# Optimization experiments

Hardware: AMD Instinct MI355X
Metric: run time of the kernel (lower is better)

## Reference

```python
import math
import jax, jax.numpy as jnp
import numpy as np

H = 16          # num attention heads
D = 64          # head dim
BUCKETS = 256   # position_buckets
MAX_POS = 512   # max_relative_positions
ATT_SPAN = BUCKETS  # pos_ebd_size A
SCALE_FACTOR = 3    # 1 + len(['c2p','p2c'])


def _log_bucket(rel):
    # log-bucketed relative positions (DeBERTa-v2 _make_log_bucket_position)
    mid = BUCKETS // 2
    rel = jnp.clip(rel, -MAX_POS + 1, MAX_POS - 1)
    sign = jnp.sign(rel).astype(jnp.float32)
    abs_pos = jnp.maximum(jnp.abs(rel), 1)
    log_base = math.log((MAX_POS - 1) / mid)
    log_pos = jnp.ceil(jnp.log(abs_pos.astype(jnp.float32) / mid) / log_base * (mid - 1)) + mid
    bucket = jnp.where(abs_pos < mid, abs_pos.astype(jnp.float32), log_pos) * sign
    return bucket.astype(jnp.int32)


def _rel_pos(q_len, k_len):
    q = jnp.arange(q_len, dtype=jnp.int32)
    k = jnp.arange(k_len, dtype=jnp.int32)
    return _log_bucket(q[:, None] - k[None, :])  # (Q, K)


def setup_inputs() -> dict:
    key = jax.random.key(0)
    ks = jax.random.split(key, 6)
    B, S, Hd = 4, 1024, 1024
    std = 0.02
    return {
        "hidden_states": jax.random.normal(ks[0], (B, S, Hd), jnp.float32),
        "rel_embeddings": jax.random.normal(ks[1], (2 * ATT_SPAN, Hd), jnp.float32) * std,
        "Wq": jax.random.normal(ks[2], (Hd, H * D), jnp.float32) * std,
        "bq": jnp.zeros((H * D,), jnp.float32),
        "Wk": jax.random.normal(ks[3], (Hd, H * D), jnp.float32) * std,
        "bk": jnp.zeros((H * D,), jnp.float32),
        "Wv": jax.random.normal(ks[4], (Hd, H * D), jnp.float32) * std,
        "bv": jnp.zeros((H * D,), jnp.float32),
    }


def reference(hidden_states, rel_embeddings, Wq, bq, Wk, bk, Wv, bv):
    B, S, Hd = hidden_states.shape
    A2 = 2 * ATT_SPAN

    def heads(x):  # (B,S,H*D) -> (B,H,S,D)
        return x.reshape(B, S, H, D).transpose(0, 2, 1, 3)

    q = heads(hidden_states @ Wq + bq)
    k = heads(hidden_states @ Wk + bk)
    v = heads(hidden_states @ Wv + bv)

    scale = math.sqrt(D * SCALE_FACTOR)
    scores = jnp.einsum('bhqd,bhkd->bhqk', q, k) / scale  # (B,H,S,S)

    rel = _rel_pos(S, S)  # (S,S) int32 bucketed relative ids
    # share_att_key=True: pos key/query use key_proj/query_proj
    pos_k = (rel_embeddings @ Wk + bk).reshape(A2, H, D).transpose(1, 0, 2)  # (H,2A,D)
    pos_q = (rel_embeddings @ Wq + bq).reshape(A2, H, D).transpose(1, 0, 2)  # (H,2A,D)

    # c2p: content->position
    c2p = jnp.einsum('bhqd,hkd->bhqk', q, pos_k)  # (B,H,S,2A)
    c2p_idx = jnp.clip(rel + ATT_SPAN, 0, A2 - 1)  # (S,S)
    c2p = jnp.take_along_axis(c2p, jnp.broadcast_to(c2p_idx[None, None], (B, H, S, S)), axis=-1) / scale

    # p2c: position->content
    p2c = jnp.einsum('bhkd,hqd->bhkq', k, pos_q)  # (B,H,S,2A)
    p2c_idx = jnp.clip(-rel + ATT_SPAN, 0, A2 - 1)  # (S,S)
    p2c = jnp.take_along_axis(p2c, jnp.broadcast_to(p2c_idx[None, None], (B, H, S, S)), axis=-1)
    p2c = jnp.swapaxes(p2c, -1, -2) / scale

    probs = jax.nn.softmax(scores + c2p + p2c, axis=-1)
    ctx = jnp.einsum('bhqk,bhkd->bhqd', probs, v)  # (B,H,S,D)
    return ctx.transpose(0, 2, 1, 3).reshape(B, S, H * D)
```

## Files before the change

### kernel.cpp

```cpp
#include <hip/hip_runtime.h>
#include <hip/hip_bf16.h>
#include <math.h>

typedef __attribute__((ext_vector_type(8))) short v8s;
typedef __attribute__((ext_vector_type(4))) short v4sh;
typedef __attribute__((ext_vector_type(4))) unsigned short v4us;
typedef __attribute__((ext_vector_type(4))) float v4f;
typedef __attribute__((ext_vector_type(4))) int   v4i;

#define AS1(p) ((const __attribute__((address_space(1))) void*)(p))
#define AS3(p) ((__attribute__((address_space(3))) void*)(p))

__device__ inline unsigned short f2b(float f){
  __hip_bfloat16 h = __float2bfloat16(f);
  return __builtin_bit_cast(unsigned short, h);
}
__device__ inline float b2f(unsigned short u){
  __hip_bfloat16 h = __builtin_bit_cast(__hip_bfloat16, u);
  return __bfloat162float(h);
}
__device__ inline unsigned cvtpk(float lo, float hi){
  unsigned d;
  asm("v_cvt_pk_bf16_f32 %0, %1, %2" : "=v"(d) : "v"(lo), "v"(hi));
  return d;
}

__device__ inline int bucket_id(int i){
  int r = i - 1023;
  if (r > 511) r = 511; if (r < -511) r = -511;
  float sign = (r > 0) ? 1.f : ((r < 0) ? -1.f : 0.f);
  int ap = r < 0 ? -r : r; if (ap < 1) ap = 1;
  float bucket;
  if (ap < 128) bucket = (float)ap * sign;
  else {
    float lp = ceilf(logf((float)ap / 128.f) / logf(511.f/128.f) * 127.f) + 128.f;
    bucket = lp * sign;
  }
  int idx = (int)bucket + 256;
  if (idx < 0) idx = 0; if (idx > 511) idx = 511;
  return idx;
}

__global__ __launch_bounds__(256) void pack_x(const float* __restrict__ hs,
                                              const float* __restrict__ rel,
                                              const float* __restrict__ Wq,
                                              const float* __restrict__ Wk,
                                              const float* __restrict__ Wv,
                                              unsigned short* __restrict__ X,
                                              unsigned short* __restrict__ Wt3,
                                              short* __restrict__ tab,
                                              unsigned long long* __restrict__ tab64){
  __shared__ unsigned short t[64][65];
  int blk = blockIdx.x;
  if (blk < 2304){
    const int HT8 = 4096*1024/8;
    int i8 = blk*256 + threadIdx.x;
    const float* src = (i8 < HT8) ? (hs + (size_t)i8*8) : (rel + ((size_t)i8 - HT8)*8);
    v8s o;
    #pragma unroll
    for (int j = 0; j < 8; j++) o[j] = (short)f2b(src[j]);
    *(v8s*)&X[(size_t)i8*8] = o;
    return;
  }
  if (blk < 2313){
    int i = (blk - 2304)*256 + threadIdx.x;
    if (i < 2047) tab[i] = (short)bucket_id(i);
    if (i < 2056){
      unsigned long long w = 0;
      #pragma unroll
      for (int r = 0; r < 4; r++)
        w |= (unsigned long long)(unsigned short)bucket_id(i + r) << (16*r);
      tab64[i] = w;
    }
    return;
  }
  int tb = blk - 2313;
  int wsel = tb >> 8, bx = tb & 255;
  const float* in = (wsel == 0) ? Wq : ((wsel == 1) ? Wk : Wv);
  unsigned short* outp = Wt3 + ((size_t)wsel << 20);
  int r0 = (bx >> 4) << 6, c0 = (bx & 15) << 6;
  int tx = threadIdx.x & 63, ty = threadIdx.x >> 6;
  #pragma unroll
  for (int p = 0; p < 16; p++){ int r = (p<<2)+ty; t[tx][r] = f2b(in[(size_t)(r0+r)*1024 + c0+tx]); }
  __syncthreads();
  #pragma unroll
  for (int p = 0; p < 16; p++){ int c = (p<<2)+ty; outp[(size_t)(c0+c)*1024 + r0+tx] = t[c][tx]; }
}

__global__ __launch_bounds__(256) void gemm_qkv(
    const unsigned short* __restrict__ A,
    const unsigned short* __restrict__ Bt3,
    unsigned short* __restrict__ Qa, unsigned short* __restrict__ Ka,
    unsigned short* __restrict__ VtT,
    const float* __restrict__ bq, const float* __restrict__ bk,
    const float* __restrict__ bv, float alpha_q)
{
  __shared__ unsigned short smem[2*128*64];
  unsigned short* a_tile = smem;
  unsigned short* b_tile = smem + 128*64;
  int nb = (blockIdx.x & 7)*108 + (blockIdx.x >> 3);
  int bm = nb / 24, bn = nb % 24;
  int m0 = bm << 7, n0 = bn << 7;
  int tid = threadIdx.x, lane = tid & 63, wave = tid >> 6;
  int l15 = lane & 15, lhi = lane >> 4;
  int rbase = (wave >> 1) << 6, cbase = (wave & 1) << 6;
  int crow[4], csw[4];
  #pragma unroll
  for (int u = 0; u < 4; u++){
    int ch = tid + (u << 8);
    crow[u] = ch >> 3;
    csw[u] = ((ch & 7) ^ (crow[u] & 7)) << 3;
  }
  v4f acc[4][4] = {};
  for (int kt = 0; kt < 1024; kt += 64){
    #pragma unroll
    for (int u = 0; u < 4; u++){
      int ch = tid + (u << 8);
      __builtin_amdgcn_global_load_lds(AS1(A   + (size_t)(m0 + crow[u])*1024 + kt + csw[u]),
                                       AS3(a_tile + (size_t)ch*8), 16, 0, 0);
      __builtin_amdgcn_global_load_lds(AS1(Bt3 + (size_t)(n0 + crow[u])*1024 + kt + csw[u]),
                                       AS3(b_tile + (size_t)ch*8), 16, 0, 0);
    }
    __syncthreads();
    #pragma unroll
    for (int ks = 0; ks < 2; ks++){
      v8s af[4], bfr[4];
      int kb = (ks << 2) + lhi;
      #pragma unroll
      for (int i = 0; i < 4; i++){
        int r = rbase + (i << 4) + l15;
        af[i] = *(const v8s*)&a_tile[r*64 + ((kb ^ (r & 7)) << 3)];
      }
      #pragma unroll
      for (int j = 0; j < 4; j++){
        int r = cbase + (j << 4) + l15;
        bfr[j] = *(const v8s*)&b_tile[r*64 + ((kb ^ (r & 7)) << 3)];
      }
      #pragma unroll
      for (int i = 0; i < 4; i++)
        #pragma unroll
        for (int j = 0; j < 4; j++)
          acc[i][j] = __builtin_amdgcn_mfma_f32_16x16x32_bf16(af[i], bfr[j], acc[i][j], 0, 0, 0);
    }
    __syncthreads();
  }
  int seg = n0 >> 10;
  int nn0 = n0 & 1023;
  if (seg == 2){
    if (m0 >= 4096) return;
    int bb = m0 >> 10, s0 = m0 & 1023;
    #pragma unroll
    for (int i = 0; i < 4; i++){
      int r = rbase + (i << 4) + (lhi << 2);
      #pragma unroll
      for (int j = 0; j < 4; j++){
        int c = cbase + (j << 4) + l15;
        float bvv = bv[nn0 + c];
        #pragma unroll
        for (int rr = 0; rr < 4; rr++)
          smem[c*128 + ((r + rr) ^ ((c & 7) << 4))] = f2b(acc[i][j][rr] + bvv);
      }
    }
    __syncthreads();
    int v = tid >> 3, sc = (tid & 7) << 4;
    #pragma unroll
    for (int vb = 0; vb < 4; vb++){
      int vv = v + (vb << 5);
      #pragma unroll
      for (int c2 = 0; c2 < 2; c2++){
        int sb = sc + (c2 << 3);
        v8s val = *(const v8s*)&smem[vv*128 + (sb ^ ((vv & 7) << 4))];
        *(v8s*)&VtT[((size_t)(bb << 10) + nn0 + vv)*1024 + s0 + sb] = val;
      }
    }
    return;
  }
  unsigned short* C = (seg == 0) ? Qa : Ka;
  const float* bias = (seg == 0) ? bq : bk;
  float alpha = (seg == 0) ? alpha_q : 1.f;
  #pragma unroll
  for (int i = 0; i < 4; i++){
    int row = rbase + (i << 4) + (lhi << 2);
    #pragma unroll
    for (int j = 0; j < 4; j++){
      int col = cbase + (j << 4) + l15;
      float bvv = bias[nn0 + col];
      #pragma unroll
      for (int r = 0; r < 4; r++)
        smem[(row + r)*128 + (col ^ (((row + r) & 7) << 4))] = f2b((acc[i][j][r] + bvv) * alpha);
    }
  }
  __syncthreads();
  #pragma unroll
  for (int c = 0; c < 8; c++){
    int row = (tid >> 4) + (c << 4);
    int col8 = (tid & 15) << 3;
    v8s val = *(const v8s*)&smem[row*128 + (col8 ^ ((row & 7) << 4))];
    *(v8s*)&C[(size_t)(m0 + row)*1024 + nn0 + col8] = val;
  }
}

__global__ __launch_bounds__(256) void gemm_pos(
    const unsigned short* __restrict__ Qa,
    const unsigned short* __restrict__ Ka,
    unsigned short* __restrict__ C2P,
    unsigned short* __restrict__ P2C)
{
  __shared__ unsigned short smem[2*128*64];
  unsigned short* a_tile = smem;
  unsigned short* b_tile = smem + 128*64;
  int tab = blockIdx.y >> 4, h = blockIdx.y & 15;
  int bm = blockIdx.x >> 2, bn = blockIdx.x & 3;
  int m0 = bm << 7, n0 = bn << 7;
  const unsigned short* A  = tab ? Ka : Qa;
  const unsigned short* Bt = tab ? Qa : Ka;
  unsigned short* C = tab ? P2C : C2P;
  int tid = threadIdx.x, lane = tid & 63, wave = tid >> 6;
  int l15 = lane & 15, lhi = lane >> 4;
  int rbase = (wave >> 1) << 6, cbase = (wave & 1) << 6;
  #pragma unroll
  for (int u = 0; u < 4; u++){
    int ch = tid + (u << 8);
    int row = ch >> 3;
    int csw = ((ch & 7) ^ (row & 7)) << 3;
    __builtin_amdgcn_global_load_lds(AS1(A  + (size_t)(m0 + row)*1024 + (h << 6) + csw),
                                     AS3(a_tile + (size_t)ch*8), 16, 0, 0);
    __builtin_amdgcn_global_load_lds(AS1(Bt + (size_t)(4096 + n0 + row)*1024 + (h << 6) + csw),
                                     AS3(b_tile + (size_t)ch*8), 16, 0, 0);
  }
  __syncthreads();
  v4f acc[4][4] = {};
  #pragma unroll
  for (int ks = 0; ks < 2; ks++){
    v8s af[4], bfr[4];
    int kb = (ks << 2) + lhi;
    #pragma unroll
    for (int i = 0; i < 4; i++){
      int r = rbase + (i << 4) + l15;
      af[i] = *(const v8s*)&a_tile[r*64 + ((kb ^ (r & 7)) << 3)];
    }
    #pragma unroll
    for (int j = 0; j < 4; j++){
      int r = cbase + (j << 4) + l15;
      bfr[j] = *(const v8s*)&b_tile[r*64 + ((kb ^ (r & 7)) << 3)];
    }
    #pragma unroll
    for (int i = 0; i < 4; i++)
      #pragma unroll
      for (int j = 0; j < 4; j++)
        acc[i][j] = __builtin_amdgcn_mfma_f32_16x16x32_bf16(af[i], bfr[j], acc[i][j], 0, 0, 0);
  }
  __syncthreads();
  #pragma unroll
  for (int i = 0; i < 4; i++){
    int row = rbase + (i << 4) + (lhi << 2);
    #pragma unroll
    for (int j = 0; j < 4; j++){
      int col = cbase + (j << 4) + l15;
      #pragma unroll
      for (int r = 0; r < 4; r++)
        smem[(row + r)*128 + (col ^ (((row + r) & 7) << 4))] = f2b(acc[i][j][r]);
    }
  }
  __syncthreads();
  #pragma unroll
  for (int c = 0; c < 8; c++){
    int row = (tid >> 4) + (c << 4);
    int col8 = (tid & 15) << 3;
    v8s val = *(const v8s*)&smem[row*128 + (col8 ^ ((row & 7) << 4))];
    *(v8s*)&C[(size_t)(m0 + row)*8192 + (h << 9) + n0 + col8] = val;
  }
}

__global__ __launch_bounds__(256) void attn(
  const unsigned short* __restrict__ Qall,
  const unsigned short* __restrict__ Kall,
  const unsigned short* __restrict__ Vt,
  const unsigned short* __restrict__ c2p,
  const unsigned short* __restrict__ p2c,
  const short* __restrict__ idxt,
  const unsigned long long* __restrict__ t64g,
  float* __restrict__ out)
{
  __shared__ unsigned short k_lds[64*64];
  __shared__ unsigned short v_lds[64*64];
  __shared__ unsigned short cw[64*72];
  __shared__ unsigned short pw[64*72];
  __shared__ short basc[16*64];
  __shared__ short basp[16*64];

  int bid = blockIdx.x;
  int xcd = bid & 7, jj = bid >> 3;
  int bh = (xcd << 3) + (jj >> 4), qb = jj & 15;
  int b = bh >> 4, h = bh & 15;
  int q0 = qb << 6;
  int tid = threadIdx.x, lane = tid & 63, wave = tid >> 6;
  int l15 = lane & 15, lhi = lane >> 4;

  #pragma unroll
  for (int v = 0; v < 8; v++){
    int i = tid + (v << 8);
    int kt = (i >> 6) & 15, row = i & 63;
    if (i < 1024){
      int bc = idxt[q0 + row - (kt << 6) + 960] & ~7;
      basc[(kt << 6) + row] = (short)(row*72 - bc);
    } else {
      int bp = idxt[q0 + 1023 - (kt << 6) - row] & ~7;
      basp[(kt << 6) + row] = (short)(row*72 - bp);
    }
  }

  int qrow = q0 + (wave << 4) + l15;
  v8s aq[2];
  #pragma unroll
  for (int ks = 0; ks < 2; ks++)
    aq[ks] = *(const v8s*)&Qall[(size_t)((b << 10) + qrow)*1024 + (h << 6) + (ks << 5) + (lhi << 3)];

  int prow_[3], pcc_[3]; bool pval[3];
  #pragma unroll
  for (int u = 0; u < 3; u++){
    int pp = tid + (u << 8);
    pval[u] = pp < 576;
    prow_[u] = pp / 9; pcc_[u] = pp - prow_[u]*9;
  }
  const size_t cbase0 = ((size_t)((b << 10) + q0))*8192 + (h << 9);
  const size_t pbase0 = ((size_t)(b << 10))*8192 + (h << 9);

  unsigned long long t64u[4];

  auto issue_kwin = [&](int kt){
    int k0 = kt << 6;
    #pragma unroll
    for (int u = 0; u < 2; u++){
      int ch = tid + (u << 8);
      int rr = ch >> 3, seg = ch & 7;
      int csw = (seg ^ (rr & 7)) << 3;
      __builtin_amdgcn_global_load_lds(AS1(Kall + (size_t)((b << 10) + k0 + rr)*1024 + (h << 6) + csw),
                                       AS3(k_lds + (size_t)ch*8), 16, 0, 0);
    }
    #pragma unroll
    for (int u = 0; u < 3; u++){
      if (pval[u]){
        int row = prow_[u], cc = pcc_[u];
        int bc = row*72 - (int)basc[(kt << 6) + row];
        __builtin_amdgcn_global_load_lds(AS1(c2p + cbase0 + (size_t)row*8192 + bc + (cc << 3)),
                                         AS3(cw + (size_t)(tid + (u << 8))*8), 16, 0, 0);
      int bp = row*72 - (int)basp[(kt << 6) + row];
        __builtin_amdgcn_global_load_lds(AS1(p2c + pbase0 + (size_t)(k0 + row)*8192 + bp + (cc << 3)),
                                         AS3(pw + (size_t)(tid + (u << 8))*8), 16, 0, 0);
      }
    }
  };
  auto issue_tv = [&](int kt){
    int k0 = kt << 6;
    int Bc = q0 - k0 + (wave << 4) + l15 - (lhi << 2) + 1020;
    #pragma unroll
    for (int j = 0; j < 4; j++) t64u[j] = t64g[Bc - (j << 4)];
    __builtin_amdgcn_sched_barrier(0);
    #pragma unroll
    for (int u = 0; u < 2; u++){
      int ch = tid + (u << 8);
      int rr = ch >> 3, seg = ch & 7;
      int csw = (seg ^ (rr & 7)) << 3;
      __builtin_amdgcn_global_load_lds(AS1(Vt + (size_t)((b << 10) + (h << 6) + rr)*1024 + k0 + csw),
                                       AS3(v_lds + (size_t)ch*8), 16, 0, 0);
    }
  };

  v4f o_acc[4] = {};
  float m_run = -INFINITY, l_part = 0.f;

  __syncthreads();
  issue_kwin(0);
  __builtin_amdgcn_sched_barrier(0);
  issue_tv(0);

  for (int kt = 0; kt < 16; kt++){
    asm volatile("s_waitcnt vmcnt(6)" ::: "memory");
    __builtin_amdgcn_sched_barrier(0);
    __builtin_amdgcn_s_barrier();
    __builtin_amdgcn_sched_barrier(0);

    v4f s_acc[4] = {};
    #pragma unroll
    for (int j = 0; j < 4; j++){
      int krow = (j << 4) + l15;
      #pragma unroll
      for (int ks = 0; ks < 2; ks++){
        v8s kf = *(const v8s*)&k_lds[krow*64 + ((((ks << 2) + lhi) ^ (krow & 7)) << 3)];
        s_acc[j] = __builtin_amdgcn_mfma_f32_16x16x32_bf16(kf, aq[ks], s_acc[j], 0, 0, 0);
      }
    }
    int cvq = (int)basc[(kt << 6) + (wave << 4) + l15];
    #pragma unroll
    for (int j = 0; j < 4; j++){
      v4sh bp4 = *(const v4sh*)&basp[(kt << 6) + (j << 4) + (lhi << 2)];
      v4us idv = __builtin_bit_cast(v4us, t64u[j]);
      #pragma unroll
      for (int r = 0; r < 4; r++){
        int id = (int)idv[3 - r];
        s_acc[j][r] += b2f(cw[cvq + id]) + b2f(pw[(int)bp4[r] + id]);
      }
    }
    float lmax = s_acc[0][0];
    #pragma unroll
    for (int j = 0; j < 4; j++)
      #pragma unroll
      for (int r = 0; r < 4; r++) lmax = fmaxf(lmax, s_acc[j][r]);
    if (__any(lmax > m_run + 6.f)){
      float mx = lmax;
      mx = fmaxf(mx, __shfl_xor(mx, 16));
      mx = fmaxf(mx, __shfl_xor(mx, 32));
      float mnew = fmaxf(m_run, mx);
      float corr = exp2f(m_run - mnew);
      m_run = mnew;
      l_part *= corr;
      float co[4];
      #pragma unroll
      for (int r = 0; r < 4; r++) co[r] = __shfl(corr, (lhi << 2) + r);
      #pragma unroll
      for (int j = 0; j < 4; j++)
        #pragma unroll
        for (int r = 0; r < 4; r++) o_acc[j][r] *= co[r];
    }
    unsigned wj[4][2];
    float ps = 0.f;
    #pragma unroll
    for (int j = 0; j < 4; j++){
      float p0 = exp2f(s_acc[j][0] - m_run);
      float p1 = exp2f(s_acc[j][1] - m_run);
      float p2 = exp2f(s_acc[j][2] - m_run);
      float p3 = exp2f(s_acc[j][3] - m_run);
      ps += (p0 + p1) + (p2 + p3);
      wj[j][0] = cvtpk(p0, p1);
      wj[j][1] = cvtpk(p2, p3);
    }
    l_part += ps;
    #pragma unroll
    for (int p = 0; p < 2; p++){
      asm("v_permlane32_swap_b32 %0, %1" : "+v"(wj[0][p]), "+v"(wj[1][p]));
      asm("v_permlane32_swap_b32 %0, %1" : "+v"(wj[2][p]), "+v"(wj[3][p]));
      asm("v_permlane16_swap_b32 %0, %1" : "+v"(wj[0][p]), "+v"(wj[1][p]));
      asm("v_permlane16_swap_b32 %0, %1" : "+v"(wj[2][p]), "+v"(wj[3][p]));
    }
    v4i pai0 = { (int)wj[0][0], (int)wj[0][1], (int)wj[1][0], (int)wj[1][1] };
    v4i pai1 = { (int)wj[2][0], (int)wj[2][1], (int)wj[3][0], (int)wj[3][1] };
    v8s pa0 = __builtin_bit_cast(v8s, pai0);
    v8s pa1 = __builtin_bit_cast(v8s, pai1);

    asm volatile("s_waitcnt vmcnt(0)" ::: "memory");
    __builtin_amdgcn_sched_barrier(0);
    __builtin_amdgcn_s_barrier();
    __builtin_amdgcn_sched_barrier(0);

    if (kt < 15) issue_kwin(kt + 1);
    __builtin_amdgcn_sched_barrier(0);

    #pragma unroll
    for (int j = 0; j < 4; j++){
      int vrow = (j << 4) + l15;
      v8s vb0 = *(const v8s*)&v_lds[vrow*64 + (((lhi) ^ (vrow & 7)) << 3)];
      o_acc[j] = __builtin_amdgcn_mfma_f32_16x16x32_bf16(pa0, vb0, o_acc[j], 0, 0, 0);
      v8s vb1 = *(const v8s*)&v_lds[vrow*64 + (((4 + lhi) ^ (vrow & 7)) << 3)];
      o_acc[j] = __builtin_amdgcn_mfma_f32_16x16x32_bf16(pa1, vb1, o_acc[j], 0, 0, 0);
    }
    if (kt < 15){
      asm volatile("s_waitcnt lgkmcnt(0)" ::: "memory");
      __builtin_amdgcn_sched_barrier(0);
      __builtin_amdgcn_s_barrier();
      __builtin_amdgcn_sched_barrier(0);
      issue_tv(kt + 1);
    }
  }
  float ls = l_part;
  ls += __shfl_xor(ls, 16);
  ls += __shfl_xor(ls, 32);
  float inv = 1.f / ls;
  float io[4];
  #pragma unroll
  for (int r = 0; r < 4; r++) io[r] = __shfl(inv, (lhi << 2) + r);
  #pragma unroll
  for (int r = 0; r < 4; r++){
    int row = q0 + (wave << 4) + (lhi << 2) + r;
    #pragma unroll
    for (int j = 0; j < 4; j++)
      out[(size_t)((b << 10) + row)*1024 + (h << 6) + (j << 4) + l15] = o_acc[j][r] * io[r];
  }
}

extern "C" void kernel_launch(void* const* d_in, const int* in_sizes, int n_in,
                              void* d_out, int out_size, void* d_ws, size_t ws_size,
                              hipStream_t stream)
{
  const float* hs  = (const float*)d_in[0];
  const float* rel = (const float*)d_in[1];
  const float* Wq  = (const float*)d_in[2];
  const float* bq  = (const float*)d_in[3];
  const float* Wk  = (const float*)d_in[4];
  const float* bk  = (const float*)d_in[5];
  const float* Wv  = (const float*)d_in[6];
  const float* bv  = (const float*)d_in[7];
  float* out = (float*)d_out;

  char* ws = (char*)d_ws;
  size_t off = 0;
  auto alloc = [&](size_t bytes) -> void* {
    void* p = ws + off; off += (bytes + 255) & ~(size_t)255; return p;
  };
  short*              idxt  = (short*)             alloc(2047 * 2);
  unsigned long long* tab64 = (unsigned long long*)alloc(2056 * 8);
  unsigned short* Xb   = (unsigned short*)alloc((size_t)4608*1024*2);
  unsigned short* Wt3  = (unsigned short*)alloc((size_t)3072*1024*2);
  unsigned short* Qa   = (unsigned short*)alloc((size_t)4608*1024*2);
  unsigned short* Ka   = (unsigned short*)alloc((size_t)4608*1024*2);
  unsigned short* VtT  = (unsigned short*)alloc((size_t)4096*1024*2);
  unsigned short* C2P  = (unsigned short*)alloc((size_t)4096*8192*2);
  unsigned short* P2C  = (unsigned short*)alloc((size_t)4096*8192*2);
  (void)                                  alloc(4096);
  (void)ws_size; (void)in_sizes; (void)n_in; (void)out_size;

  pack_x<<<3081, 256, 0, stream>>>(hs, rel, Wq, Wk, Wv, Xb, Wt3, idxt, tab64);

  const float alpha_q = 1.4426950408889634f / sqrtf(192.f);
  gemm_qkv<<<864, 256, 0, stream>>>(Xb, Wt3, Qa, Ka, VtT, bq, bk, bv, alpha_q);

  gemm_pos<<<dim3(128, 32), 256, 0, stream>>>(Qa, Ka, C2P, P2C);

  attn<<<1024, 256, 0, stream>>>(Qa, Ka, VtT, C2P, P2C, idxt, tab64, out);
}
```

Measured before the change: 158.5 us.

## Skip unused pos-GEMM tiles, widen attention blocks to 128 queries, double-buffer V

gemm_pos now returns early for output tiles whose columns fall outside the bucket-index range that the attention kernel will read, and its block order is remapped across XCDs. The attention kernel moves to 512 threads covering 128 query rows, so each K/V tile and p2c window is shared by twice as many queries. V is double-buffered so its load for the next step is issued together with the K/c2p/p2c loads, which removes one barrier per iteration. MFMA sections are wrapped with s_setprio. The risks are lower occupancy from the larger LDS footprint and fewer blocks, plus correctness depending on the skip bounds derived from idxt.

```diff
diff --git a/kernel.cpp b/kernel.cpp
--- a/kernel.cpp
+++ b/kernel.cpp
@@ -203,15 +203,24 @@
 __global__ __launch_bounds__(256) void gemm_pos(
     const unsigned short* __restrict__ Qa,
     const unsigned short* __restrict__ Ka,
+    const short* __restrict__ idxt,
     unsigned short* __restrict__ C2P,
     unsigned short* __restrict__ P2C)
 {
   __shared__ unsigned short smem[2*128*64];
   unsigned short* a_tile = smem;
   unsigned short* b_tile = smem + 128*64;
+  int xs = (blockIdx.x & 7)*16 + (blockIdx.x >> 3);
   int tab = blockIdx.y >> 4, h = blockIdx.y & 15;
-  int bm = blockIdx.x >> 2, bn = blockIdx.x & 3;
+  int bm = xs >> 2, bn = xs & 3;
   int m0 = bm << 7, n0 = bn << 7;
+  {
+    int s0 = m0 & 1023;
+    int lo, hi;
+    if (tab == 0){ lo = idxt[s0];       hi = idxt[s0 + 1150]; }
+    else         { lo = idxt[896 - s0]; hi = idxt[2046 - s0]; }
+    if (n0 > hi + 7 || n0 + 127 < (lo & ~7)) return;
+  }
   const unsigned short* A  = tab ? Ka : Qa;
   const unsigned short* Bt = tab ? Qa : Ka;
   unsigned short* C = tab ? P2C : C2P;
@@ -272,7 +281,7 @@
   }
 }
 
-__global__ __launch_bounds__(256) void attn(
+__global__ __launch_bounds__(512) void attn(
   const unsigned short* __restrict__ Qall,
   const unsigned short* __restrict__ Kall,
   const unsigned short* __restrict__ Vt,
@@ -283,30 +292,32 @@
   float* __restrict__ out)
 {
   __shared__ unsigned short k_lds[64*64];
-  __shared__ unsigned short v_lds[64*64];
-  __shared__ unsigned short cw[64*72];
-  __shared__ unsigned short pw[64*72];
-  __shared__ short basc[16*64];
+  __shared__ unsigned short v_lds[2][64*64];
+  __shared__ unsigned short cw[128*72];
+  __shared__ unsigned short pw[64*152];
+  __shared__ short basc[16*128];
   __shared__ short basp[16*64];
 
   int bid = blockIdx.x;
   int xcd = bid & 7, jj = bid >> 3;
-  int bh = (xcd << 3) + (jj >> 4), qb = jj & 15;
+  int bh = (xcd << 3) + (jj >> 3), qb = jj & 7;
   int b = bh >> 4, h = bh & 15;
-  int q0 = qb << 6;
+  int q0 = qb << 7;
   int tid = threadIdx.x, lane = tid & 63, wave = tid >> 6;
   int l15 = lane & 15, lhi = lane >> 4;
 
   #pragma unroll
-  for (int v = 0; v < 8; v++){
-    int i = tid + (v << 8);
-    int kt = (i >> 6) & 15, row = i & 63;
-    if (i < 1024){
+  for (int v = 0; v < 6; v++){
+    int i = tid + (v << 9);
+    if (i < 2048){
+      int kt = i >> 7, row = i & 127;
       int bc = idxt[q0 + row - (kt << 6) + 960] & ~7;
-      basc[(kt << 6) + row] = (short)(row*72 - bc);
-    } else {
+      basc[i] = (short)(row*72 - bc);
+    } else if (i < 3072){
+      int i2 = i - 2048;
+      int kt = i2 >> 6, row = i2 & 63;
       int bp = idxt[q0 + 1023 - (kt << 6) - row] & ~7;
-      basp[(kt << 6) + row] = (short)(row*72 - bp);
+      basp[i2] = (short)(row*152 - bp);
     }
   }
 
@@ -316,13 +327,6 @@
   for (int ks = 0; ks < 2; ks++)
     aq[ks] = *(const v8s*)&Qall[(size_t)((b << 10) + qrow)*1024 + (h << 6) + (ks << 5) + (lhi << 3)];
 
-  int prow_[3], pcc_[3]; bool pval[3];
-  #pragma unroll
-  for (int u = 0; u < 3; u++){
-    int pp = tid + (u << 8);
-    pval[u] = pp < 576;
-    prow_[u] = pp / 9; pcc_[u] = pp - prow_[u]*9;
-  }
   const size_t cbase0 = ((size_t)((b << 10) + q0))*8192 + (h << 9);
   const size_t pbase0 = ((size_t)(b << 10))*8192 + (h << 9);
 
@@ -330,40 +334,44 @@
 
   auto issue_kwin = [&](int kt){
     int k0 = kt << 6;
-    #pragma unroll
-    for (int u = 0; u < 2; u++){
-      int ch = tid + (u << 8);
-      int rr = ch >> 3, seg = ch & 7;
+    {
+      int rr = tid >> 3, seg = tid & 7;
       int csw = (seg ^ (rr & 7)) << 3;
       __builtin_amdgcn_global_load_lds(AS1(Kall + (size_t)((b << 10) + k0 + rr)*1024 + (h << 6) + csw),
-                                       AS3(k_lds + (size_t)ch*8), 16, 0, 0);
+                                       AS3(k_lds + (size_t)tid*8), 16, 0, 0);
     }
     #pragma unroll
     for (int u = 0; u < 3; u++){
-      if (pval[u]){
-        int row = prow_[u], cc = pcc_[u];
-        int bc = row*72 - (int)basc[(kt << 6) + row];
+      int pp = tid + (u << 9);
+      if (pp < 1152){
+        int row = pp / 9, cc = pp - row*9;
+        int bc = row*72 - (int)basc[(kt << 7) + row];
         __builtin_amdgcn_global_load_lds(AS1(c2p + cbase0 + (size_t)row*8192 + bc + (cc << 3)),
-                                         AS3(cw + (size_t)(tid + (u << 8))*8), 16, 0, 0);
-      int bp = row*72 - (int)basp[(kt << 6) + row];
+                                         AS3(cw + (size_t)pp*8), 16, 0, 0);
+      }
+    }
+    #pragma unroll
+    for (int u = 0; u < 3; u++){
+      int pp = tid + (u << 9);
+      if (pp < 1152){
+        int row = pp / 18, cc = pp - row*18;
+        int bp = row*152 - (int)basp[(kt << 6) + row];
         __builtin_amdgcn_global_load_lds(AS1(p2c + pbase0 + (size_t)(k0 + row)*8192 + bp + (cc << 3)),
-                                         AS3(pw + (size_t)(tid + (u << 8))*8), 16, 0, 0);
+                                         AS3(pw + (size_t)(row*152 + (cc << 3))), 16, 0, 0);
       }
     }
   };
-  auto issue_tv = [&](int kt){
+  auto issue_tv = [&](int kt, int sel){
     int k0 = kt << 6;
     int Bc = q0 - k0 + (wave << 4) + l15 - (lhi << 2) + 1020;
     #pragma unroll
     for (int j = 0; j < 4; j++) t64u[j] = t64g[Bc - (j << 4)];
     __builtin_amdgcn_sched_barrier(0);
-    #pragma unroll
-    for (int u = 0; u < 2; u++){
-      int ch = tid + (u << 8);
-      int rr = ch >> 3, seg = ch & 7;
+    {
+      int rr = tid >> 3, seg = tid & 7;
       int csw = (seg ^ (rr & 7)) << 3;
       __builtin_amdgcn_global_load_lds(AS1(Vt + (size_t)((b << 10) + (h << 6) + rr)*1024 + k0 + csw),
-                                       AS3(v_lds + (size_t)ch*8), 16, 0, 0);
+                                       AS3(&v_lds[sel][0] + (size_t)tid*8), 16, 0, 0);
     }
   };
 
@@ -373,15 +381,16 @@
   __syncthreads();
   issue_kwin(0);
   __builtin_amdgcn_sched_barrier(0);
-  issue_tv(0);
+  issue_tv(0, 0);
 
   for (int kt = 0; kt < 16; kt++){
-    asm volatile("s_waitcnt vmcnt(6)" ::: "memory");
+    asm volatile("s_waitcnt vmcnt(5)" ::: "memory");
     __builtin_amdgcn_sched_barrier(0);
     __builtin_amdgcn_s_barrier();
     __builtin_amdgcn_sched_barrier(0);
 
     v4f s_acc[4] = {};
+    __builtin_amdgcn_s_setprio(1);
     #pragma unroll
     for (int j = 0; j < 4; j++){
       int krow = (j << 4) + l15;
@@ -391,7 +400,8 @@
         s_acc[j] = __builtin_amdgcn_mfma_f32_16x16x32_bf16(kf, aq[ks], s_acc[j], 0, 0, 0);
       }
     }
-    int cvq = (int)basc[(kt << 6) + (wave << 4) + l15];
+    __builtin_amdgcn_s_setprio(0);
+    int cvq = (int)basc[(kt << 7) + (wave << 4) + l15];
     #pragma unroll
     for (int j = 0; j < 4; j++){
       v4sh bp4 = *(const v4sh*)&basp[(kt << 6) + (j << 4) + (lhi << 2)];
@@ -453,24 +463,24 @@
     __builtin_amdgcn_s_barrier();
     __builtin_amdgcn_sched_barrier(0);
 
-    if (kt < 15) issue_kwin(kt + 1);
-    __builtin_amdgcn_sched_barrier(0);
-
+    if (kt < 15){
+      issue_kwin(kt + 1);
+      __builtin_amdgcn_sched_barrier(0);
+      issue_tv(kt + 1, (kt + 1) & 1);
+      __builtin_amdgcn_sched_barrier(0);
+    }
+
+    const unsigned short* vl = &v_lds[kt & 1][0];
+    __builtin_amdgcn_s_setprio(1);
     #pragma unroll
     for (int j = 0; j < 4; j++){
       int vrow = (j << 4) + l15;
-      v8s vb0 = *(const v8s*)&v_lds[vrow*64 + (((lhi) ^ (vrow & 7)) << 3)];
+      v8s vb0 = *(const v8s*)&vl[vrow*64 + (((lhi) ^ (vrow & 7)) << 3)];
+      v8s vb1 = *(const v8s*)&vl[vrow*64 + (((4 + lhi) ^ (vrow & 7)) << 3)];
       o_acc[j] = __builtin_amdgcn_mfma_f32_16x16x32_bf16(pa0, vb0, o_acc[j], 0, 0, 0);
-      v8s vb1 = *(const v8s*)&v_lds[vrow*64 + (((4 + lhi) ^ (vrow & 7)) << 3)];
       o_acc[j] = __builtin_amdgcn_mfma_f32_16x16x32_bf16(pa1, vb1, o_acc[j], 0, 0, 0);
     }
-    if (kt < 15){
-      asm volatile("s_waitcnt lgkmcnt(0)" ::: "memory");
-      __builtin_amdgcn_sched_barrier(0);
-      __builtin_amdgcn_s_barrier();
-      __builtin_amdgcn_sched_barrier(0);
-      issue_tv(kt + 1);
-    }
+    __builtin_amdgcn_s_setprio(0);
   }
   float ls = l_part;
   ls += __shfl_xor(ls, 16);
@@ -524,7 +534,7 @@
   const float alpha_q = 1.4426950408889634f / sqrtf(192.f);
   gemm_qkv<<<864, 256, 0, stream>>>(Xb, Wt3, Qa, Ka, VtT, bq, bk, bv, alpha_q);
 
-  gemm_pos<<<dim3(128, 32), 256, 0, stream>>>(Qa, Ka, C2P, P2C);
-
-  attn<<<1024, 256, 0, stream>>>(Qa, Ka, VtT, C2P, P2C, idxt, tab64, out);
-}
+  gemm_pos<<<dim3(128, 32), 256, 0, stream>>>(Qa, Ka, idxt, C2P, P2C);
+
+  attn<<<512, 512, 0, stream>>>(Qa, Ka, VtT, C2P, P2C, idxt, tab64, out);
+}
```

After: 147.4 us. -7.0%, faster.
